# Kernel optimization log

Hardware: AMD Instinct MI355X
Metric: run time of the kernel (lower is better)

## Reference

```python
import jax, jax.numpy as jnp
import numpy as np

NUM_HEADS = 12
HEAD_DIM = 64
HIDDEN = NUM_HEADS * HEAD_DIM


def setup_inputs() -> dict:
    key = jax.random.key(0)
    ks = jax.random.split(key, 10)
    B, S, N_ROT = 8, 1374, 1369
    s = 0.02
    return {
        "hidden_states": jax.random.normal(ks[0], (B, S, HIDDEN), jnp.float32),
        "sin": jax.random.normal(ks[1], (N_ROT, HEAD_DIM), jnp.float32),
        "cos": jax.random.normal(ks[2], (N_ROT, HEAD_DIM), jnp.float32),
        "Wq": jax.random.normal(ks[3], (HIDDEN, HIDDEN), jnp.float32) * s,
        "bq": jax.random.normal(ks[4], (HIDDEN,), jnp.float32) * s,
        "Wk": jax.random.normal(ks[5], (HIDDEN, HIDDEN), jnp.float32) * s,
        "Wv": jax.random.normal(ks[6], (HIDDEN, HIDDEN), jnp.float32) * s,
        "bv": jax.random.normal(ks[7], (HIDDEN,), jnp.float32) * s,
        "Wp": jax.random.normal(ks[8], (HIDDEN, HIDDEN), jnp.float32) * s,
        "bp": jax.random.normal(ks[9], (HIDDEN,), jnp.float32) * s,
    }


def _rotate_half(x):
    x1, x2 = jnp.split(x, 2, axis=-1)
    return jnp.concatenate([-x2, x1], axis=-1)


def _rope_apply(x, sin, cos):
    return x * cos + _rotate_half(x) * sin


def reference(hidden_states, sin, cos, Wq, bq, Wk, Wv, bv, Wp, bp):
    B, S, _ = hidden_states.shape
    scaling = HEAD_DIM ** -0.5

    def to_heads(x):  # [B,S,HIDDEN] -> [B,H,S,D]
        return x.reshape(B, S, NUM_HEADS, HEAD_DIM).transpose(0, 2, 1, 3)

    q = to_heads(hidden_states @ Wq.T + bq)
    k = to_heads(hidden_states @ Wk.T)  # no key bias (mask_k_bias)
    v = to_heads(hidden_states @ Wv.T + bv)

    # RoPE only on patch tokens (prefix = cls + register tokens untouched)
    prefix = S - sin.shape[-2]
    q = jnp.concatenate([q[:, :, :prefix], _rope_apply(q[:, :, prefix:], sin, cos)], axis=2)
    k = jnp.concatenate([k[:, :, :prefix], _rope_apply(k[:, :, prefix:], sin, cos)], axis=2)

    # eager attention: softmax in float32, no mask, no dropout (eval)
    scores = jnp.einsum("bhqd,bhkd->bhqk", q, k) * scaling
    probs = jax.nn.softmax(scores.astype(jnp.float32), axis=-1).astype(q.dtype)
    ctx = jnp.einsum("bhqk,bhkd->bqhd", probs, v).reshape(B, S, HIDDEN)
    return ctx @ Wp.T + bp
```

## Files before the change

kernel.cpp:

```cpp
#include <hip/hip_runtime.h>
#include <stdint.h>

typedef unsigned short u16;
typedef unsigned int u32;
typedef u16 u16x8 __attribute__((ext_vector_type(8)));
typedef __bf16 bf16x8 __attribute__((ext_vector_type(8)));
typedef float f32x4 __attribute__((ext_vector_type(4)));

#define S_LEN 1374
#define S_PAD 1408
#define PRE_TOK 5
#define HID 768
#define NH 12
#define MPAD 11008

__device__ __forceinline__ u16 f2bf(float f) {
    union { float f; u32 u; } v; v.f = f;
    u32 r = v.u + 0x7fffu + ((v.u >> 16) & 1u);
    return (u16)(r >> 16);
}
__device__ __forceinline__ bf16x8 as_bf(u16x8 v) { bf16x8 r; __builtin_memcpy(&r, &v, 16); return r; }
__device__ __forceinline__ bf16x8 lds_load8(const u16* p) {
    u16x8 t = *(const u16x8*)p;
    return as_bf(t);
}
__device__ __forceinline__ u32 cvtpk_bf16(float lo, float hi) {
    u32 r;
    asm("v_cvt_pk_bf16_f32 %0, %1, %2" : "=v"(r) : "v"(lo), "v"(hi));
    return r;
}
__device__ __forceinline__ float fexp2(float x) {
    float r;
    asm("v_exp_f32 %0, %1" : "=v"(r) : "v"(x));
    return r;
}
__device__ __forceinline__ void gload16(void* lds, const void* g) {
    unsigned int __attribute__((address_space(1)))* gp =
        (unsigned int __attribute__((address_space(1)))*)(unsigned long long)g;
    unsigned int __attribute__((address_space(3)))* lp =
        (unsigned int __attribute__((address_space(3)))*)(unsigned int)(unsigned long long)lds;
    __builtin_amdgcn_global_load_lds(gp, lp, 16, 0, 0);
}
__device__ __forceinline__ int xcd_swz(int orig, int nwg) {
    int qd = nwg >> 3, rd = nwg & 7;
    int xcd = orig & 7, rem = orig >> 3;
    return (xcd < rd ? xcd * (qd + 1) : rd * (qd + 1) + (xcd - rd) * qd) + rem;
}


__global__ __launch_bounds__(256) void pack_xw(
    const float* __restrict__ X, const float* __restrict__ Wq, const float* __restrict__ Wk,
    const float* __restrict__ Wv, const float* __restrict__ Wp, const float* __restrict__ bq,
    const float* __restrict__ bv, u16* __restrict__ Xb,
    u16* __restrict__ wqkv, u16* __restrict__ wpb, float* __restrict__ bqkv)
{
    int bid = blockIdx.x;
    int tid = threadIdx.x;
    if (bid < 4128) {
        size_t i = (size_t)bid * 256 + tid;
        size_t e = i * 8;
        const size_t TOT = (size_t)10992 * HID;
        u16x8 o = {0,0,0,0,0,0,0,0};
        if (e < TOT) {
            f32x4 a = *(const f32x4*)(X + e);
            f32x4 b = *(const f32x4*)(X + e + 4);
#pragma unroll
            for (int j = 0; j < 4; ++j) { o[j] = f2bf(a[j]); o[4 + j] = f2bf(b[j]); }
        }
        *(u16x8*)(Xb + e) = o;
        return;
    }
    int g = (bid - 4128) * 256 + tid;
    const int QKV8 = 2304 * HID / 8;
    const int P8 = HID * HID / 8;
    if (g < QKV8) {
        int e = g * 8;
        int row = e / HID, col = e - row * HID;
        const float* src = (row < 768) ? (Wq + (size_t)row * HID + col)
                         : (row < 1536) ? (Wk + (size_t)(row - 768) * HID + col)
                                        : (Wv + (size_t)(row - 1536) * HID + col);
        u16x8 o;
#pragma unroll
        for (int j = 0; j < 8; ++j) o[j] = f2bf(src[j]);
        *(u16x8*)(wqkv + e) = o;
    } else if (g < QKV8 + P8) {
        int e = (g - QKV8) * 8;
        u16x8 o;
#pragma unroll
        for (int j = 0; j < 8; ++j) o[j] = f2bf(Wp[e + j]);
        *(u16x8*)(wpb + e) = o;
    }
    if (g < 288) {
        int e = g * 8;
#pragma unroll
        for (int j = 0; j < 8; ++j) {
            int c = e + j;
            bqkv[c] = (c < 768) ? bq[c] : (c < 1536 ? 0.f : bv[c - 1536]);
        }
    }
}


template <int EPI>
__global__ __launch_bounds__(512) void gemm_nt(
    const u16* __restrict__ A, const u16* __restrict__ B, const float* __restrict__ bias,
    float* __restrict__ Yf, u16* __restrict__ Qh, u16* __restrict__ Kh,
    u16* __restrict__ Yv, const float* __restrict__ SN, const float* __restrict__ CS,
    int N, int K, int nx, int nwg)
{
    __shared__ u16 As[128 * 64];
    __shared__ u16 Bs[256 * 64];
    int tid = threadIdx.x;
    int w = tid >> 6, l = tid & 63;
    int fr = l & 15, fg = l >> 4;
    int wg = xcd_swz(blockIdx.x, nwg);
    int col0 = (wg % nx) * 256;
    int row0 = (wg / nx) * 128;
    int wr = (w >> 2) * 64;
    int wc = (w & 3) * 64;

    f32x4 zero4 = {0.f, 0.f, 0.f, 0.f};
    f32x4 acc[4][4];
#pragma unroll
    for (int m = 0; m < 4; ++m)
#pragma unroll
        for (int n = 0; n < 4; ++n) acc[m][n] = zero4;

    int arow[2], aoff[2];
#pragma unroll
    for (int i = 0; i < 2; ++i) {
        int sbyte = (i * 512 + tid) * 16;
        int r = sbyte >> 7;
        int ir = (sbyte & 127) ^ ((r & 7) << 4);
        arow[i] = r; aoff[i] = ir >> 1;
    }
    int brow[4], boff[4];
#pragma unroll
    for (int i = 0; i < 4; ++i) {
        int sbyte = (i * 512 + tid) * 16;
        int r = sbyte >> 7;
        int ir = (sbyte & 127) ^ ((r & 7) << 4);
        brow[i] = r; boff[i] = ir >> 1;
    }

    for (int kt = 0; kt < K; kt += 64) {
#pragma unroll
        for (int i = 0; i < 2; ++i)
            gload16((char*)As + i * 8192 + w * 1024,
                    A + (size_t)(row0 + arow[i]) * K + kt + aoff[i]);
#pragma unroll
        for (int i = 0; i < 4; ++i)
            gload16((char*)Bs + i * 8192 + w * 1024,
                    B + (size_t)(col0 + brow[i]) * K + kt + boff[i]);
        __syncthreads();
#pragma unroll
        for (int c = 0; c < 2; ++c) {
            bf16x8 af[4], bfr[4];
#pragma unroll
            for (int m = 0; m < 4; ++m) {
                int r = wr + m * 16 + fr;
                int byte_ = (c * 64 + fg * 16) ^ ((r & 7) << 4);
                af[m] = lds_load8(As + r * 64 + (byte_ >> 1));
            }
#pragma unroll
            for (int n = 0; n < 4; ++n) {
                int r = wc + n * 16 + fr;
                int byte_ = (c * 64 + fg * 16) ^ ((r & 7) << 4);
                bfr[n] = lds_load8(Bs + r * 64 + (byte_ >> 1));
            }
#pragma unroll
            for (int m = 0; m < 4; ++m)
#pragma unroll
                for (int n = 0; n < 4; ++n)
                    acc[m][n] = __builtin_amdgcn_mfma_f32_16x16x32_bf16(af[m], bfr[n], acc[m][n], 0, 0, 0);
        }
        __syncthreads();
    }

    if (EPI == 1) {
#pragma unroll
        for (int m = 0; m < 4; ++m)
#pragma unroll
            for (int n = 0; n < 4; ++n) {
                int gn = col0 + wc + n * 16 + fr;
                float bvv = bias[gn];
#pragma unroll
                for (int j = 0; j < 4; ++j) {
                    int gm = row0 + wr + m * 16 + fg * 4 + j;
                    if (gm < 10992) Yf[(size_t)gm * N + gn] = acc[m][n][j] + bvv;
                }
            }
    } else {
        int sect = col0 >= 1536 ? 2 : (col0 >= 768 ? 1 : 0);
        if (sect == 2) {
#pragma unroll
            for (int m = 0; m < 4; ++m)
#pragma unroll
                for (int n = 0; n < 4; ++n) {
                    int gn = col0 + wc + n * 16 + fr;
                    float bvv = bias[gn];
#pragma unroll
                    for (int j = 0; j < 4; ++j) {
                        int gm = row0 + wr + m * 16 + fg * 4 + j;
                        if (gm < 10992)
                            Yv[(size_t)gm * HID + (gn - 1536)] = f2bf(acc[m][n][j] + bvv);
                    }
                }
        } else {
            u16* H = sect ? Kh : Qh;
            const float QS = sect ? 1.f : 0.125f * 1.44269504088896f;
            int hh = ((col0 + wc) >> 6) - sect * NH;
            float bv4[4];
#pragma unroll
            for (int n = 0; n < 4; ++n) bv4[n] = bias[col0 + wc + n * 16 + fr];
#pragma unroll
            for (int m = 0; m < 4; ++m)
#pragma unroll
                for (int j = 0; j < 4; ++j) {
                    int gm = row0 + wr + m * 16 + fg * 4 + j;
                    if (gm < 10992) {
                        int b = gm / 1374, s = gm - b * 1374;
                        size_t ob = ((size_t)(b * NH + hh) * S_PAD + s) * 64;
#pragma unroll
                        for (int n2 = 0; n2 < 2; ++n2) {
                            int d = n2 * 16 + fr;
                            float v1 = acc[m][n2][j] + bv4[n2];
                            float v2 = acc[m][n2 + 2][j] + bv4[n2 + 2];
                            float a1 = v1, a2 = v2;
                            if (s >= PRE_TOK) {
                                size_t rr = (size_t)(s - PRE_TOK) * 64;
                                float c1 = CS[rr + d], s1 = SN[rr + d];
                                float c2 = CS[rr + d + 32], s2 = SN[rr + d + 32];
                                a1 = v1 * c1 - v2 * s1;
                                a2 = v2 * c2 + v1 * s2;
                            }
                            H[ob + d]      = f2bf(a1 * QS);
                            H[ob + d + 32] = f2bf(a2 * QS);
                        }
                    }
                }
        }
    }
}


__global__ __launch_bounds__(256) void v_pack(const u16* __restrict__ Yv, u16* __restrict__ Vt) {
    int st = blockIdx.x, bh = blockIdx.y;
    int b = bh / NH, h = bh - b * NH;
    int tid = threadIdx.x;
    int sl = tid >> 2, dg = (tid & 3) * 8;
    int s = st * 64 + sl;
    __shared__ u16 vtile[64 * 64];

    u16x8 a = {0,0,0,0,0,0,0,0}, a2 = {0,0,0,0,0,0,0,0};
    if (s < S_LEN) {
        size_t base = ((size_t)b * S_LEN + s) * HID + h * 64;
        a  = *(const u16x8*)(Yv + base + dg);
        a2 = *(const u16x8*)(Yv + base + 32 + dg);
    }
#pragma unroll
    for (int j = 0; j < 8; ++j) {
        vtile[(dg + j) * 64 + sl] = a[j];
        vtile[(32 + dg + j) * 64 + sl] = a2[j];
    }
    __syncthreads();
    int d = tid >> 2, so = (tid & 3) * 8;
    u16x8 ov0 = *(const u16x8*)(vtile + d * 64 + so);
    u16x8 ov1 = *(const u16x8*)(vtile + d * 64 + so + 32);
    size_t vrow = ((size_t)bh * 64 + d) * S_PAD + st * 64;
    *(u16x8*)(Vt + vrow + so) = ov0;
    *(u16x8*)(Vt + vrow + so + 32) = ov1;
}


#define FLASH_B64(Kc, Vc, KsN, VsN, ktn, DO_STAGE, DO_MASK)                           \
    {                                                                                 \
        asm volatile("s_waitcnt vmcnt(0) lgkmcnt(0)" ::: "memory");                   \
        __syncthreads();                                                              \
        if (DO_STAGE) {                                                               \
            int k0n = (ktn) * 64;                                                     \
            _Pragma("unroll")                                                         \
            for (int i = 0; i < 2; ++i) {                                             \
                gload16((char*)(KsN) + i * 4096 + w * 1024, Kb + (size_t)k0n * 64 + kfix[i]); \
                gload16((char*)(VsN) + i * 4096 + w * 1024, Vb + (size_t)k0n + vfix[i]);      \
            }                                                                         \
        }                                                                             \
        _Pragma("unroll")                                                             \
        for (int h = 0; h < 2; ++h) {                                                 \
            f32x4 sf[2][2];                                                           \
            __builtin_amdgcn_s_setprio(1);                                            \
            _Pragma("unroll")                                                         \
            for (int n = 0; n < 2; ++n) {                                             \
                f32x4 q0a = zero4, q1a = zero4;                                       \
                _Pragma("unroll")                                                     \
                for (int c = 0; c < 2; ++c) {                                         \
                    int byte_ = (c * 64 + fg * 16) ^ ((fr & 7) << 4);                 \
                    bf16x8 kf = lds_load8((Kc) + (h * 32 + n * 16 + fr) * 64 + (byte_ >> 1)); \
                    q0a = __builtin_amdgcn_mfma_f32_16x16x32_bf16(kf, qf[0][c], q0a, 0, 0, 0); \
                    q1a = __builtin_amdgcn_mfma_f32_16x16x32_bf16(kf, qf[1][c], q1a, 0, 0, 0); \
                }                                                                     \
                sf[0][n] = q0a; sf[1][n] = q1a;                                       \
            }                                                                         \
            __builtin_amdgcn_s_setprio(0);                                            \
            if (DO_MASK) {                                                            \
                _Pragma("unroll")                                                     \
                for (int n = 0; n < 2; ++n)                                           \
                    _Pragma("unroll")                                                 \
                    for (int j = 0; j < 4; ++j)                                       \
                        if (1344 + h * 32 + 8 * fg + 4 * n + j >= S_LEN) {            \
                            sf[0][n][j] = -1e30f; sf[1][n][j] = -1e30f;               \
                        }                                                             \
            }                                                                         \
            union PA { u32 w2[4]; bf16x8 v; } pa[2];                                  \
            _Pragma("unroll")                                                         \
            for (int qq = 0; qq < 2; ++qq) {                                          \
                _Pragma("unroll")                                                     \
                for (int n = 0; n < 2; ++n)                                           \
                    _Pragma("unroll")                                                 \
                    for (int j = 0; j < 4; ++j) sf[qq][n][j] = fexp2(sf[qq][n][j]);   \
                pa[qq].w2[0] = cvtpk_bf16(sf[qq][0][0], sf[qq][0][1]);                \
                pa[qq].w2[1] = cvtpk_bf16(sf[qq][0][2], sf[qq][0][3]);                \
                pa[qq].w2[2] = cvtpk_bf16(sf[qq][1][0], sf[qq][1][1]);                \
                pa[qq].w2[3] = cvtpk_bf16(sf[qq][1][2], sf[qq][1][3]);                \
            }                                                                         \
            __builtin_amdgcn_s_setprio(1);                                            \
            lsum0 = __builtin_amdgcn_mfma_f32_16x16x32_bf16(pa[0].v, ones, lsum0, 0, 0, 0); \
            lsum1 = __builtin_amdgcn_mfma_f32_16x16x32_bf16(pa[1].v, ones, lsum1, 0, 0, 0); \
            _Pragma("unroll")                                                         \
            for (int nd = 0; nd < 4; ++nd) {                                          \
                int byte_ = (h * 64 + fg * 16) ^ ((fr & 7) << 4);                     \
                bf16x8 vf = lds_load8((Vc) + (nd * 16 + fr) * 64 + (byte_ >> 1));     \
                octx[0][nd] = __builtin_amdgcn_mfma_f32_16x16x32_bf16(pa[0].v, vf, octx[0][nd], 0, 0, 0); \
                octx[1][nd] = __builtin_amdgcn_mfma_f32_16x16x32_bf16(pa[1].v, vf, octx[1][nd], 0, 0, 0); \
            }                                                                         \
            __builtin_amdgcn_s_setprio(0);                                            \
        }                                                                             \
    }

__global__ __launch_bounds__(256, 4) void flash(
    const u16* __restrict__ Qh, const u16* __restrict__ Kh, const u16* __restrict__ Vt,
    u16* __restrict__ ctxO)
{
    int wg = (blockIdx.x & 7) * 132 + (blockIdx.x >> 3);
    int qt = wg % 11, bh = wg / 11;
    int b = bh / NH, h = bh - b * NH;
    int q0 = qt * 128;
    int tid = threadIdx.x, w = tid >> 6, l = tid & 63;
    int fr = l & 15, fg = l >> 4;

    __shared__ u16 Ks0[64 * 64], Ks1[64 * 64];
    __shared__ u16 Vs0[64 * 64], Vs1[64 * 64];

    const u16* Qb = Qh + (size_t)bh * S_PAD * 64;
    const u16* Kb = Kh + (size_t)bh * S_PAD * 64;
    const u16* Vb = Vt + (size_t)bh * 64 * S_PAD;

    bf16x8 qf[2][2];
#pragma unroll
    for (int qq = 0; qq < 2; ++qq) {
        int qrow = q0 + w * 32 + qq * 16 + fr;
#pragma unroll
        for (int c = 0; c < 2; ++c)
            qf[qq][c] = as_bf(*(const u16x8*)(Qb + (size_t)qrow * 64 + c * 32 + fg * 8));
    }

    u16x8 ones_u = {0x3F80, 0x3F80, 0x3F80, 0x3F80, 0x3F80, 0x3F80, 0x3F80, 0x3F80};
    bf16x8 ones = as_bf(ones_u);

    f32x4 zero4 = {0.f, 0.f, 0.f, 0.f};
    f32x4 octx[2][4];
#pragma unroll
    for (int qq = 0; qq < 2; ++qq)
#pragma unroll
        for (int nd = 0; nd < 4; ++nd) octx[qq][nd] = zero4;
    f32x4 lsum0 = zero4, lsum1 = zero4;

    int kfix[2], vfix[2];
#pragma unroll
    for (int i = 0; i < 2; ++i) {
        int sby = (i * 256 + tid) * 16;
        int r = sby >> 7;
        int ir = (sby & 127) ^ ((r & 7) << 4);
        int r5 = r & 31;
        int gk = (r >> 5) * 32 + 8 * ((r5 >> 2) & 3) + 4 * (r5 >> 4) + (r5 & 3);
        kfix[i] = gk * 64 + (ir >> 1);
        vfix[i] = r * S_PAD + (ir >> 1);
    }

    {
#pragma unroll
        for (int i = 0; i < 2; ++i) {
            gload16((char*)Ks0 + i * 4096 + w * 1024, Kb + kfix[i]);
            gload16((char*)Vs0 + i * 4096 + w * 1024, Vb + vfix[i]);
        }
    }

    for (int kt = 0; kt < 20; kt += 2) {
        FLASH_B64(Ks0, Vs0, Ks1, Vs1, kt + 1, true, false);
        FLASH_B64(Ks1, Vs1, Ks0, Vs0, kt + 2, true, false);
    }
    FLASH_B64(Ks0, Vs0, Ks1, Vs1, 21, true, false);
    FLASH_B64(Ks1, Vs1, Ks0, Vs0, 0, false, true);

#pragma unroll
    for (int qq = 0; qq < 2; ++qq)
#pragma unroll
        for (int j = 0; j < 4; ++j) {
            int q = q0 + w * 32 + qq * 16 + fg * 4 + j;
            if (q < S_LEN) {
                float lv = qq ? lsum1[j] : lsum0[j];
                float inv = 1.f / lv;
                size_t rowb = ((size_t)b * S_LEN + q) * HID + h * 64;
#pragma unroll
                for (int nd = 0; nd < 4; ++nd)
                    ctxO[rowb + nd * 16 + fr] = f2bf(octx[qq][nd][j] * inv);
            }
        }
}


extern "C" void kernel_launch(void* const* d_in, const int* in_sizes, int n_in,
                              void* d_out, int out_size, void* d_ws, size_t ws_size,
                              hipStream_t stream) {
    (void)in_sizes; (void)n_in; (void)out_size; (void)ws_size;
    const float* X  = (const float*)d_in[0];
    const float* SN = (const float*)d_in[1];
    const float* CS = (const float*)d_in[2];
    const float* Wq = (const float*)d_in[3];
    const float* bq = (const float*)d_in[4];
    const float* Wk = (const float*)d_in[5];
    const float* Wv = (const float*)d_in[6];
    const float* bv = (const float*)d_in[7];
    const float* Wp = (const float*)d_in[8];
    const float* bp = (const float*)d_in[9];
    float* OUT = (float*)d_out;
    char* ws = (char*)d_ws;

    u16*   xb   = (u16*)(ws);
    u16*   wqkv = (u16*)(ws + 16908288);
    u16*   wpb  = (u16*)(ws + 20447232);
    float* bqkv = (float*)(ws + 21626880);
    u16*   Yv   = (u16*)(ws + 21636096);
    u16*   Qh   = (u16*)(ws + 72360960);
    u16*   Kh   = (u16*)(ws + 89662464);
    u16*   Vt   = (u16*)(ws + 106963968);
    u16*   ctx  = xb;

    pack_xw<<<5280, 256, 0, stream>>>(X, Wq, Wk, Wv, Wp, bq, bv, xb, wqkv, wpb, bqkv);
    gemm_nt<2><<<774, 512, 0, stream>>>(xb, wqkv, bqkv, nullptr, Qh, Kh, Yv, SN, CS, 2304, 768, 9, 774);
    v_pack<<<dim3(22, 96), 256, 0, stream>>>(Yv, Vt);
    flash<<<1056, 256, 0, stream>>>(Qh, Kh, Vt, ctx);
    gemm_nt<1><<<258, 512, 0, stream>>>(ctx, wpb, bp, OUT, nullptr, nullptr, nullptr, nullptr, nullptr, 768, 768, 3, 258);
}
```

Measured before the change: 166.3 us.

## Fuse V transpose into QKV GEMM epilogue and drop v_pack kernel

The V section of the QKV GEMM epilogue now stages the bf16 tile in shared memory with an XOR swizzle and writes it transposed directly into the head-major Vt layout. This removes the separate v_pack kernel and the round trip of the intermediate Yv buffer through global memory. A memset of Vt is added to zero the padding, and the epilogue gains extra barriers plus a slow scalar path for rows that cross a batch boundary.

```diff
diff --git a/kernel.cpp b/kernel.cpp
--- a/kernel.cpp
+++ b/kernel.cpp
@@ -105,7 +105,7 @@
 __global__ __launch_bounds__(512) void gemm_nt(
     const u16* __restrict__ A, const u16* __restrict__ B, const float* __restrict__ bias,
     float* __restrict__ Yf, u16* __restrict__ Qh, u16* __restrict__ Kh,
-    u16* __restrict__ Yv, const float* __restrict__ SN, const float* __restrict__ CS,
+    u16* __restrict__ Vt, const float* __restrict__ SN, const float* __restrict__ CS,
     int N, int K, int nx, int nwg)
 {
     __shared__ u16 As[128 * 64];
@@ -193,19 +193,57 @@
     } else {
         int sect = col0 >= 1536 ? 2 : (col0 >= 768 ? 1 : 0);
         if (sect == 2) {
-#pragma unroll
-            for (int m = 0; m < 4; ++m)
-#pragma unroll
-                for (int n = 0; n < 4; ++n) {
-                    int gn = col0 + wc + n * 16 + fr;
-                    float bvv = bias[gn];
-#pragma unroll
-                    for (int j = 0; j < 4; ++j) {
-                        int gm = row0 + wr + m * 16 + fg * 4 + j;
-                        if (gm < 10992)
-                            Yv[(size_t)gm * HID + (gn - 1536)] = f2bf(acc[m][n][j] + bvv);
+            int p_own = (w & 3) >> 1;
+            int head2 = w & 1;
+            int hbase = (col0 - 1536) >> 6;
+            u16* Lt = Bs;
+            float bv4[4];
+#pragma unroll
+            for (int n = 0; n < 4; ++n) bv4[n] = bias[col0 + wc + n * 16 + fr];
+#pragma unroll
+            for (int p = 0; p < 2; ++p) {
+                __syncthreads();
+                if (p_own == p) {
+#pragma unroll
+                    for (int m = 0; m < 4; ++m)
+#pragma unroll
+                        for (int n = 0; n < 4; ++n) {
+                            int d = n * 16 + fr;
+#pragma unroll
+                            for (int j = 0; j < 4; ++j) {
+                                int t = wr + m * 16 + fg * 4 + j;
+                                int eb = ((head2 * 8192 + d * 128 + t) * 2) ^ ((d & 7) << 4);
+                                *(u16*)((char*)Lt + eb) = f2bf(acc[m][n][j] + bv4[n]);
+                            }
+                        }
+                }
+                __syncthreads();
+#pragma unroll
+                for (int sw = 0; sw < 4; ++sw) {
+                    int e = sw * 4096 + tid * 8;
+                    int h2 = e >> 13;
+                    int rem = e & 8191;
+                    int d = rem >> 7;
+                    int t0 = rem & 127;
+                    int eb = (e * 2) ^ ((d & 7) << 4);
+                    u16x8 v = *(const u16x8*)((char*)Lt + eb);
+                    int gm = row0 + t0;
+                    if (gm < 10992) {
+                        int b2 = gm / 1374, s0 = gm - b2 * 1374;
+                        int hh = hbase + p * 2 + h2;
+                        if (s0 + 8 <= 1374) {
+                            *(u16x8*)(Vt + ((size_t)(b2 * NH + hh) * 64 + d) * S_PAD + s0) = v;
+                        } else {
+#pragma unroll
+                            for (int j = 0; j < 8; ++j) {
+                                int gmj = gm + j;
+                                int bj = gmj / 1374, sj = gmj - bj * 1374;
+                                Vt[((size_t)(bj * NH + hh) * 64 + d) * S_PAD + sj] = v[j];
+                            }
+                        }
                     }
                 }
+            }
         } else {
             u16* H = sect ? Kh : Qh;
             const float QS = sect ? 1.f : 0.125f * 1.44269504088896f;
@@ -241,35 +279,6 @@
                 }
         }
     }
-}
-
-
-__global__ __launch_bounds__(256) void v_pack(const u16* __restrict__ Yv, u16* __restrict__ Vt) {
-    int st = blockIdx.x, bh = blockIdx.y;
-    int b = bh / NH, h = bh - b * NH;
-    int tid = threadIdx.x;
-    int sl = tid >> 2, dg = (tid & 3) * 8;
-    int s = st * 64 + sl;
-    __shared__ u16 vtile[64 * 64];
-
-    u16x8 a = {0,0,0,0,0,0,0,0}, a2 = {0,0,0,0,0,0,0,0};
-    if (s < S_LEN) {
-        size_t base = ((size_t)b * S_LEN + s) * HID + h * 64;
-        a  = *(const u16x8*)(Yv + base + dg);
-        a2 = *(const u16x8*)(Yv + base + 32 + dg);
-    }
-#pragma unroll
-    for (int j = 0; j < 8; ++j) {
-        vtile[(dg + j) * 64 + sl] = a[j];
-        vtile[(32 + dg + j) * 64 + sl] = a2[j];
-    }
-    __syncthreads();
-    int d = tid >> 2, so = (tid & 3) * 8;
-    u16x8 ov0 = *(const u16x8*)(vtile + d * 64 + so);
-    u16x8 ov1 = *(const u16x8*)(vtile + d * 64 + so + 32);
-    size_t vrow = ((size_t)bh * 64 + d) * S_PAD + st * 64;
-    *(u16x8*)(Vt + vrow + so) = ov0;
-    *(u16x8*)(Vt + vrow + so + 32) = ov1;
 }
 
 
@@ -440,15 +449,14 @@
     u16*   wqkv = (u16*)(ws + 16908288);
     u16*   wpb  = (u16*)(ws + 20447232);
     float* bqkv = (float*)(ws + 21626880);
-    u16*   Yv   = (u16*)(ws + 21636096);
     u16*   Qh   = (u16*)(ws + 72360960);
     u16*   Kh   = (u16*)(ws + 89662464);
     u16*   Vt   = (u16*)(ws + 106963968);
     u16*   ctx  = xb;
 
+    hipMemsetAsync(Vt, 0, (size_t)96 * 64 * S_PAD * 2, stream);
     pack_xw<<<5280, 256, 0, stream>>>(X, Wq, Wk, Wv, Wp, bq, bv, xb, wqkv, wpb, bqkv);
-    gemm_nt<2><<<774, 512, 0, stream>>>(xb, wqkv, bqkv, nullptr, Qh, Kh, Yv, SN, CS, 2304, 768, 9, 774);
-    v_pack<<<dim3(22, 96), 256, 0, stream>>>(Yv, Vt);
+    gemm_nt<2><<<774, 512, 0, stream>>>(xb, wqkv, bqkv, nullptr, Qh, Kh, Vt, SN, CS, 2304, 768, 9, 774);
     flash<<<1056, 256, 0, stream>>>(Qh, Kh, Vt, ctx);
     gemm_nt<1><<<258, 512, 0, stream>>>(ctx, wpb, bp, OUT, nullptr, nullptr, nullptr, nullptr, nullptr, 768, 768, 3, 258);
 }
```

Result: no change. 168.0 us (+1.1%).
